# Kernel optimization log

Hardware: AMD Instinct MI355X
Metric: run time of the kernel (lower is better)

Reference implementation:

```python
import jax, jax.numpy as jnp
import numpy as np

B, S, DM, H = 4, 4096, 1024, 16
HD = DM // H  # 64


def setup_inputs() -> dict:
    key = jax.random.key(0)
    ks = jax.random.split(key, 9)
    sc = 0.02
    x = jax.random.normal(ks[0], (B, S, DM), dtype=jnp.float32)
    Wq = jax.random.normal(ks[1], (DM, DM), dtype=jnp.float32) * sc
    bq = jnp.zeros((DM,), dtype=jnp.float32)
    Wk = jax.random.normal(ks[2], (DM, HD), dtype=jnp.float32) * sc
    bk = jnp.zeros((HD,), dtype=jnp.float32)
    Wv = jax.random.normal(ks[3], (DM, HD), dtype=jnp.float32) * sc
    bv = jnp.zeros((HD,), dtype=jnp.float32)
    Wo = jax.random.normal(ks[4], (DM, DM), dtype=jnp.float32) * sc
    bo = jnp.zeros((DM,), dtype=jnp.float32)
    return {"x": x, "Wq": Wq, "bq": bq, "Wk": Wk, "bk": bk,
            "Wv": Wv, "bv": bv, "Wo": Wo, "bo": bo}


def reference(x, Wq, bq, Wk, bk, Wv, bv, Wo, bo):
    b, s, _ = x.shape
    q = (x @ Wq + bq).reshape(b, s, H, HD)          # [B,S,H,D]
    k = (x @ Wk + bk)                                # [B,S,D] (single KV head)
    v = (x @ Wv + bv)                                # [B,S,D]
    # Faithful to source: k/v expanded over head axis, matmul over last two
    # dims of [B,S,H,D] -> scores are per-token head-vs-head: [B,S,H,H].
    k_e = jnp.broadcast_to(k[:, :, None, :], (b, s, H, HD))
    v_e = jnp.broadcast_to(v[:, :, None, :], (b, s, H, HD))
    scores = jnp.einsum('bshd,bsgd->bshg', q, k_e) / jnp.sqrt(jnp.float32(HD))
    attn = jax.nn.softmax(scores, axis=-1)           # uniform (scores const over g)
    out = jnp.einsum('bshg,bsgd->bshd', attn, v_e)   # [B,S,H,D]
    return out.reshape(b, s, DM) @ Wo + bo
```

## Files before the change

### kernel.cpp

```cpp
#include <hip/hip_runtime.h>

#define M_TOTAL 16384
#define DMODEL  1024
#define HDIM    64
#define NHEAD   16

typedef _Float16 half8 __attribute__((ext_vector_type(8)));
typedef float    f32x4 __attribute__((ext_vector_type(4)));

__global__ __launch_bounds__(256) void prep_kernel(const float* __restrict__ Wv,
                                                   const float* __restrict__ Wo,
                                                   _Float16* __restrict__ WvT,
                                                   _Float16* __restrict__ WosumT) {
    const int t = blockIdx.x * 256 + threadIdx.x;
    {
        const int d = t & 63, k = t >> 6;
        WvT[d * DMODEL + k] = (_Float16)Wv[k * HDIM + d];
    }
    {
        const int n = t & 1023, d = t >> 10;
        float s = 0.f;
        #pragma unroll
        for (int h = 0; h < NHEAD; ++h) s += Wo[(h * HDIM + d) * DMODEL + n];
        WosumT[n * HDIM + d] = (_Float16)s;
    }
}

__global__ __launch_bounds__(256) void vproj_kernel(const float* __restrict__ X,
                                                    const float* __restrict__ bv,
                                                    const _Float16* __restrict__ WvT,
                                                    _Float16* __restrict__ V) {
    const int tid = threadIdx.x;
    const int l   = tid & 63;
    const int w   = tid >> 6;
    const int lr  = l & 15;
    const int lk  = l >> 4;
    const int m0  = (blockIdx.x * 4 + w) * 16;

    const float* xrow = X + (size_t)(m0 + lr) * DMODEL + lk * 8;

    f32x4 acc[4] = {};
    float4 abuf[4][2];
    #pragma unroll
    for (int s = 0; s < 4; ++s) {
        abuf[s][0] = *(const float4*)(xrow + s * 32);
        abuf[s][1] = *(const float4*)(xrow + s * 32 + 4);
    }
    #pragma unroll 4
    for (int s = 0; s < 32; ++s) {
        const int slot = s & 3;
        const float4 x0 = abuf[slot][0];
        const float4 x1 = abuf[slot][1];
        if (s < 28) {
            abuf[slot][0] = *(const float4*)(xrow + (s + 4) * 32);
            abuf[slot][1] = *(const float4*)(xrow + (s + 4) * 32 + 4);
        }
        union { _Float16 h[8]; half8 v; } pk;
        pk.h[0] = (_Float16)x0.x; pk.h[1] = (_Float16)x0.y;
        pk.h[2] = (_Float16)x0.z; pk.h[3] = (_Float16)x0.w;
        pk.h[4] = (_Float16)x1.x; pk.h[5] = (_Float16)x1.y;
        pk.h[6] = (_Float16)x1.z; pk.h[7] = (_Float16)x1.w;
        #pragma unroll
        for (int n4 = 0; n4 < 4; ++n4) {
            const half8 b = *(const half8*)&WvT[(size_t)(n4 * 16 + lr) * DMODEL + s * 32 + lk * 8];
            acc[n4] = __builtin_amdgcn_mfma_f32_16x16x32_f16(pk.v, b, acc[n4], 0, 0, 0);
        }
    }
    #pragma unroll
    for (int n4 = 0; n4 < 4; ++n4) {
        const float bvv = bv[n4 * 16 + lr];
        #pragma unroll
        for (int j = 0; j < 4; ++j)
            V[(size_t)(m0 + lk * 4 + j) * HDIM + n4 * 16 + lr] = (_Float16)(acc[n4][j] + bvv);
    }
}

__global__ __launch_bounds__(256) void oproj_kernel(const _Float16* __restrict__ V,
                                                    const float* __restrict__ bo,
                                                    const _Float16* __restrict__ WosumT,
                                                    float* __restrict__ Out) {
    const int tid = threadIdx.x;
    const int l   = tid & 63;
    const int w   = tid >> 6;
    const int lr  = l & 15;
    const int lk  = l >> 4;
    const int m0  = blockIdx.x * 16;

    const _Float16* vp = V + (size_t)(m0 + lr) * HDIM + lk * 8;
    const half8 a0 = *(const half8*)vp;
    const half8 a1 = *(const half8*)(vp + 32);

    #pragma unroll 4
    for (int nf = 0; nf < 16; ++nf) {
        const int n0 = w * 256 + nf * 16;
        const half8 b0 = *(const half8*)&WosumT[(size_t)(n0 + lr) * HDIM + lk * 8];
        const half8 b1 = *(const half8*)&WosumT[(size_t)(n0 + lr) * HDIM + 32 + lk * 8];
        f32x4 o = {};
        o = __builtin_amdgcn_mfma_f32_16x16x32_f16(a0, b0, o, 0, 0, 0);
        o = __builtin_amdgcn_mfma_f32_16x16x32_f16(a1, b1, o, 0, 0, 0);
        const float bov = bo[n0 + lr];
        #pragma unroll
        for (int j = 0; j < 4; ++j)
            Out[(size_t)(m0 + lk * 4 + j) * DMODEL + n0 + lr] = o[j] + bov;
    }
}

extern "C" void kernel_launch(void* const* d_in, const int* in_sizes, int n_in,
                              void* d_out, int out_size, void* d_ws, size_t ws_size,
                              hipStream_t stream) {
    const float* x  = (const float*)d_in[0];
    const float* Wv = (const float*)d_in[5];
    const float* bv = (const float*)d_in[6];
    const float* Wo = (const float*)d_in[7];
    const float* bo = (const float*)d_in[8];

    _Float16* WvT    = (_Float16*)d_ws;
    _Float16* WosumT = (_Float16*)((char*)d_ws + 64 * 1024 * 2);
    _Float16* V      = (_Float16*)((char*)d_ws + 256 * 1024);
    float*    out    = (float*)d_out;

    prep_kernel<<<256, 256, 0, stream>>>(Wv, Wo, WvT, WosumT);
    vproj_kernel<<<M_TOTAL / 64, 256, 0, stream>>>(x, bv, WvT, V);
    oproj_kernel<<<M_TOTAL / 16, 256, 0, stream>>>(V, bo, WosumT, out);
}
```

Before: 62.03 us.

## Split V-projection K dimension across waves and blocks with atomic reduction

Result: slower. 72.70 us (+17.2%).

```diff
diff --git a/kernel.cpp b/kernel.cpp
--- a/kernel.cpp
+++ b/kernel.cpp
@@ -11,7 +11,8 @@
 __global__ __launch_bounds__(256) void prep_kernel(const float* __restrict__ Wv,
                                                    const float* __restrict__ Wo,
                                                    _Float16* __restrict__ WvT,
-                                                   _Float16* __restrict__ WosumT) {
+                                                   _Float16* __restrict__ WosumT,
+                                                   float* __restrict__ Vg) {
     const int t = blockIdx.x * 256 + threadIdx.x;
     {
         const int d = t & 63, k = t >> 6;
@@ -24,80 +25,109 @@
         for (int h = 0; h < NHEAD; ++h) s += Wo[(h * HDIM + d) * DMODEL + n];
         WosumT[n * HDIM + d] = (_Float16)s;
     }
+    {
+        f32x4 z = {};
+        float* p = Vg + (size_t)t * 16;
+        *(f32x4*)(p) = z; *(f32x4*)(p + 4) = z;
+        *(f32x4*)(p + 8) = z; *(f32x4*)(p + 12) = z;
+    }
 }
 
-__global__ __launch_bounds__(256) void vproj_kernel(const float* __restrict__ X,
-                                                    const float* __restrict__ bv,
-                                                    const _Float16* __restrict__ WvT,
-                                                    _Float16* __restrict__ V) {
+#define VP_S 68
+
+__global__ __launch_bounds__(256, 8) void vproj_kernel(const float* __restrict__ X,
+                                                       const _Float16* __restrict__ WvT,
+                                                       float* __restrict__ Vg) {
+    __shared__ float Vp[4][16][VP_S];
+
     const int tid = threadIdx.x;
     const int l   = tid & 63;
     const int w   = tid >> 6;
     const int lr  = l & 15;
     const int lk  = l >> 4;
-    const int m0  = (blockIdx.x * 4 + w) * 16;
+    const int m0  = (blockIdx.x >> 1) * 16;
+    const int ks0 = (blockIdx.x & 1) * 512 + w * 128;
 
-    const float* xrow = X + (size_t)(m0 + lr) * DMODEL + lk * 8;
-
-    f32x4 acc[4] = {};
-    float4 abuf[4][2];
+    const float* xp = X + (size_t)(m0 + lr) * DMODEL + ks0 + lk * 8;
+    f32x4 xb[8];
     #pragma unroll
     for (int s = 0; s < 4; ++s) {
-        abuf[s][0] = *(const float4*)(xrow + s * 32);
-        abuf[s][1] = *(const float4*)(xrow + s * 32 + 4);
+        xb[2 * s]     = *(const f32x4*)(xp + s * 32);
+        xb[2 * s + 1] = *(const f32x4*)(xp + s * 32 + 4);
     }
-    #pragma unroll 4
-    for (int s = 0; s < 32; ++s) {
-        const int slot = s & 3;
-        const float4 x0 = abuf[slot][0];
-        const float4 x1 = abuf[slot][1];
-        if (s < 28) {
-            abuf[slot][0] = *(const float4*)(xrow + (s + 4) * 32);
-            abuf[slot][1] = *(const float4*)(xrow + (s + 4) * 32 + 4);
+    f32x4 acc[4] = {};
+    #pragma unroll
+    for (int s = 0; s < 4; ++s) {
+        union { _Float16 h[8]; half8 v; } pk;
+        #pragma unroll
+        for (int j = 0; j < 4; ++j) {
+            pk.h[j]     = (_Float16)xb[2 * s][j];
+            pk.h[4 + j] = (_Float16)xb[2 * s + 1][j];
         }
-        union { _Float16 h[8]; half8 v; } pk;
-        pk.h[0] = (_Float16)x0.x; pk.h[1] = (_Float16)x0.y;
-        pk.h[2] = (_Float16)x0.z; pk.h[3] = (_Float16)x0.w;
-        pk.h[4] = (_Float16)x1.x; pk.h[5] = (_Float16)x1.y;
-        pk.h[6] = (_Float16)x1.z; pk.h[7] = (_Float16)x1.w;
         #pragma unroll
         for (int n4 = 0; n4 < 4; ++n4) {
-            const half8 b = *(const half8*)&WvT[(size_t)(n4 * 16 + lr) * DMODEL + s * 32 + lk * 8];
+            const half8 b = *(const half8*)&WvT[(size_t)(n4 * 16 + lr) * DMODEL + ks0 + s * 32 + lk * 8];
             acc[n4] = __builtin_amdgcn_mfma_f32_16x16x32_f16(pk.v, b, acc[n4], 0, 0, 0);
         }
     }
     #pragma unroll
-    for (int n4 = 0; n4 < 4; ++n4) {
-        const float bvv = bv[n4 * 16 + lr];
+    for (int n4 = 0; n4 < 4; ++n4)
         #pragma unroll
         for (int j = 0; j < 4; ++j)
-            V[(size_t)(m0 + lk * 4 + j) * HDIM + n4 * 16 + lr] = (_Float16)(acc[n4][j] + bvv);
-    }
+            Vp[w][lk * 4 + j][n4 * 16 + lr] = acc[n4][j];
+    __syncthreads();
+
+    const int idx = tid * 4;
+    const int r   = idx >> 6;
+    const int c   = idx & 63;
+    f32x4 s4 = {};
+    #pragma unroll
+    for (int p = 0; p < 4; ++p) s4 += *(const f32x4*)&Vp[p][r][c];
+    float* vg = &Vg[(size_t)(m0 + r) * HDIM + c];
+    atomicAdd(vg + 0, s4[0]); atomicAdd(vg + 1, s4[1]);
+    atomicAdd(vg + 2, s4[2]); atomicAdd(vg + 3, s4[3]);
 }
 
-__global__ __launch_bounds__(256) void oproj_kernel(const _Float16* __restrict__ V,
-                                                    const float* __restrict__ bo,
-                                                    const _Float16* __restrict__ WosumT,
-                                                    float* __restrict__ Out) {
+__global__ __launch_bounds__(256, 8) void oproj_kernel(const float* __restrict__ Vg,
+                                                       const float* __restrict__ bv,
+                                                       const float* __restrict__ bo,
+                                                       const _Float16* __restrict__ WosumT,
+                                                       float* __restrict__ Out) {
     const int tid = threadIdx.x;
     const int l   = tid & 63;
     const int w   = tid >> 6;
     const int lr  = l & 15;
     const int lk  = l >> 4;
-    const int m0  = blockIdx.x * 16;
+    const int m0  = (blockIdx.x >> 1) * 16;
+    const int nb  = (blockIdx.x & 1) * 512 + w * 128;
 
-    const _Float16* vp = V + (size_t)(m0 + lr) * HDIM + lk * 8;
-    const half8 a0 = *(const half8*)vp;
-    const half8 a1 = *(const half8*)(vp + 32);
+    const float* vp = Vg + (size_t)(m0 + lr) * HDIM + lk * 8;
+    const f32x4 v0 = *(const f32x4*)(vp);
+    const f32x4 v1 = *(const f32x4*)(vp + 4);
+    const f32x4 v2 = *(const f32x4*)(vp + 32);
+    const f32x4 v3 = *(const f32x4*)(vp + 36);
+    const f32x4 b0 = *(const f32x4*)&bv[lk * 8];
+    const f32x4 b1 = *(const f32x4*)&bv[lk * 8 + 4];
+    const f32x4 b2 = *(const f32x4*)&bv[32 + lk * 8];
+    const f32x4 b3 = *(const f32x4*)&bv[32 + lk * 8 + 4];
+
+    union { _Float16 h[8]; half8 v; } A0, A1;
+    #pragma unroll
+    for (int j = 0; j < 4; ++j) {
+        A0.h[j]     = (_Float16)(v0[j] + b0[j]);
+        A0.h[4 + j] = (_Float16)(v1[j] + b1[j]);
+        A1.h[j]     = (_Float16)(v2[j] + b2[j]);
+        A1.h[4 + j] = (_Float16)(v3[j] + b3[j]);
+    }
 
     #pragma unroll 4
-    for (int nf = 0; nf < 16; ++nf) {
-        const int n0 = w * 256 + nf * 16;
-        const half8 b0 = *(const half8*)&WosumT[(size_t)(n0 + lr) * HDIM + lk * 8];
-        const half8 b1 = *(const half8*)&WosumT[(size_t)(n0 + lr) * HDIM + 32 + lk * 8];
+    for (int g = 0; g < 8; ++g) {
+        const int n0 = nb + g * 16;
+        const half8 w0 = *(const half8*)&WosumT[(size_t)(n0 + lr) * HDIM + lk * 8];
+        const half8 w1 = *(const half8*)&WosumT[(size_t)(n0 + lr) * HDIM + 32 + lk * 8];
         f32x4 o = {};
-        o = __builtin_amdgcn_mfma_f32_16x16x32_f16(a0, b0, o, 0, 0, 0);
-        o = __builtin_amdgcn_mfma_f32_16x16x32_f16(a1, b1, o, 0, 0, 0);
+        o = __builtin_amdgcn_mfma_f32_16x16x32_f16(A0.v, w0, o, 0, 0, 0);
+        o = __builtin_amdgcn_mfma_f32_16x16x32_f16(A1.v, w1, o, 0, 0, 0);
         const float bov = bo[n0 + lr];
         #pragma unroll
         for (int j = 0; j < 4; ++j)
@@ -116,10 +146,10 @@
 
     _Float16* WvT    = (_Float16*)d_ws;
     _Float16* WosumT = (_Float16*)((char*)d_ws + 64 * 1024 * 2);
-    _Float16* V      = (_Float16*)((char*)d_ws + 256 * 1024);
+    float*    Vg     = (float*)((char*)d_ws + 256 * 1024);
     float*    out    = (float*)d_out;
 
-    prep_kernel<<<256, 256, 0, stream>>>(Wv, Wo, WvT, WosumT);
-    vproj_kernel<<<M_TOTAL / 64, 256, 0, stream>>>(x, bv, WvT, V);
-    oproj_kernel<<<M_TOTAL / 16, 256, 0, stream>>>(V, bo, WosumT, out);
+    prep_kernel<<<256, 256, 0, stream>>>(Wv, Wo, WvT, WosumT, Vg);
+    vproj_kernel<<<2048, 256, 0, stream>>>(x, WvT, Vg);
+    oproj_kernel<<<2048, 256, 0, stream>>>(Vg, bv, bo, WosumT, out);
 }
```

## Split V projection K-dimension across 8 waves with LDS reduction; widen oproj grid

Applied to the files above, without the earlier changes.

New measurement: 61.64 us. Within noise of the previous version (-0.6%).

```diff
diff --git a/kernel.cpp b/kernel.cpp
--- a/kernel.cpp
+++ b/kernel.cpp
@@ -7,6 +7,7 @@
 
 typedef _Float16 half8 __attribute__((ext_vector_type(8)));
 typedef float    f32x4 __attribute__((ext_vector_type(4)));
+typedef float    f32x2 __attribute__((ext_vector_type(2)));
 
 __global__ __launch_bounds__(256) void prep_kernel(const float* __restrict__ Wv,
                                                    const float* __restrict__ Wo,
@@ -26,78 +27,101 @@
     }
 }
 
-__global__ __launch_bounds__(256) void vproj_kernel(const float* __restrict__ X,
-                                                    const float* __restrict__ bv,
-                                                    const _Float16* __restrict__ WvT,
-                                                    _Float16* __restrict__ V) {
-    const int tid = threadIdx.x;
-    const int l   = tid & 63;
-    const int w   = tid >> 6;
-    const int lr  = l & 15;
-    const int lk  = l >> 4;
-    const int m0  = (blockIdx.x * 4 + w) * 16;
+#define VP_S 68
 
-    const float* xrow = X + (size_t)(m0 + lr) * DMODEL + lk * 8;
+__global__ __launch_bounds__(512, 4) void vproj_kernel(const float* __restrict__ X,
+                                                       const float* __restrict__ bv,
+                                                       const _Float16* __restrict__ WvT,
+                                                       _Float16* __restrict__ V) {
+    __shared__ float Vp[8][16][VP_S];
 
-    f32x4 acc[4] = {};
-    float4 abuf[4][2];
-    #pragma unroll
-    for (int s = 0; s < 4; ++s) {
-        abuf[s][0] = *(const float4*)(xrow + s * 32);
-        abuf[s][1] = *(const float4*)(xrow + s * 32 + 4);
-    }
-    #pragma unroll 4
-    for (int s = 0; s < 32; ++s) {
-        const int slot = s & 3;
-        const float4 x0 = abuf[slot][0];
-        const float4 x1 = abuf[slot][1];
-        if (s < 28) {
-            abuf[slot][0] = *(const float4*)(xrow + (s + 4) * 32);
-            abuf[slot][1] = *(const float4*)(xrow + (s + 4) * 32 + 4);
-        }
-        union { _Float16 h[8]; half8 v; } pk;
-        pk.h[0] = (_Float16)x0.x; pk.h[1] = (_Float16)x0.y;
-        pk.h[2] = (_Float16)x0.z; pk.h[3] = (_Float16)x0.w;
-        pk.h[4] = (_Float16)x1.x; pk.h[5] = (_Float16)x1.y;
-        pk.h[6] = (_Float16)x1.z; pk.h[7] = (_Float16)x1.w;
-        #pragma unroll
-        for (int n4 = 0; n4 < 4; ++n4) {
-            const half8 b = *(const half8*)&WvT[(size_t)(n4 * 16 + lr) * DMODEL + s * 32 + lk * 8];
-            acc[n4] = __builtin_amdgcn_mfma_f32_16x16x32_f16(pk.v, b, acc[n4], 0, 0, 0);
-        }
-    }
-    #pragma unroll
-    for (int n4 = 0; n4 < 4; ++n4) {
-        const float bvv = bv[n4 * 16 + lr];
-        #pragma unroll
-        for (int j = 0; j < 4; ++j)
-            V[(size_t)(m0 + lk * 4 + j) * HDIM + n4 * 16 + lr] = (_Float16)(acc[n4][j] + bvv);
-    }
-}
-
-__global__ __launch_bounds__(256) void oproj_kernel(const _Float16* __restrict__ V,
-                                                    const float* __restrict__ bo,
-                                                    const _Float16* __restrict__ WosumT,
-                                                    float* __restrict__ Out) {
     const int tid = threadIdx.x;
     const int l   = tid & 63;
     const int w   = tid >> 6;
     const int lr  = l & 15;
     const int lk  = l >> 4;
     const int m0  = blockIdx.x * 16;
+    const int k0  = w * 128;
+
+    const float* xp = X + (size_t)(m0 + lr) * DMODEL + k0 + lk * 8;
+    f32x4 xb[8];
+    #pragma unroll
+    for (int s = 0; s < 4; ++s) {
+        xb[2 * s]     = *(const f32x4*)(xp + s * 32);
+        xb[2 * s + 1] = *(const f32x4*)(xp + s * 32 + 4);
+    }
+    half8 Bf[4][4];
+    #pragma unroll
+    for (int n4 = 0; n4 < 4; ++n4)
+        #pragma unroll
+        for (int s = 0; s < 4; ++s)
+            Bf[n4][s] = *(const half8*)&WvT[(size_t)(n4 * 16 + lr) * DMODEL + k0 + s * 32 + lk * 8];
+
+    f32x4 acc[4] = {};
+    #pragma unroll
+    for (int s = 0; s < 4; ++s) {
+        union { _Float16 h[8]; half8 v; } pk;
+        #pragma unroll
+        for (int j = 0; j < 4; ++j) {
+            pk.h[j]     = (_Float16)xb[2 * s][j];
+            pk.h[4 + j] = (_Float16)xb[2 * s + 1][j];
+        }
+        #pragma unroll
+        for (int n4 = 0; n4 < 4; ++n4)
+            acc[n4] = __builtin_amdgcn_mfma_f32_16x16x32_f16(pk.v, Bf[n4][s], acc[n4], 0, 0, 0);
+    }
+    #pragma unroll
+    for (int n4 = 0; n4 < 4; ++n4)
+        #pragma unroll
+        for (int j = 0; j < 4; ++j)
+            Vp[w][lk * 4 + j][n4 * 16 + lr] = acc[n4][j];
+    __syncthreads();
+
+    const int idx = tid * 2;
+    const int r   = idx >> 6;
+    const int c   = idx & 63;
+    f32x2 s2 = {};
+    #pragma unroll
+    for (int p = 0; p < 8; ++p) s2 += *(const f32x2*)&Vp[p][r][c];
+    s2 += *(const f32x2*)&bv[c];
+    union { _Float16 h[2]; unsigned int u; } o;
+    o.h[0] = (_Float16)s2[0];
+    o.h[1] = (_Float16)s2[1];
+    *(unsigned int*)&V[(size_t)(m0 + r) * HDIM + c] = o.u;
+}
+
+__global__ __launch_bounds__(256, 8) void oproj_kernel(const _Float16* __restrict__ V,
+                                                       const float* __restrict__ bo,
+                                                       const _Float16* __restrict__ WosumT,
+                                                       float* __restrict__ Out) {
+    const int tid = threadIdx.x;
+    const int l   = tid & 63;
+    const int w   = tid >> 6;
+    const int lr  = l & 15;
+    const int lk  = l >> 4;
+    const int m0  = (blockIdx.x >> 1) * 16;
+    const int nb  = (blockIdx.x & 1) * 512 + w * 128;
 
     const _Float16* vp = V + (size_t)(m0 + lr) * HDIM + lk * 8;
     const half8 a0 = *(const half8*)vp;
     const half8 a1 = *(const half8*)(vp + 32);
 
-    #pragma unroll 4
-    for (int nf = 0; nf < 16; ++nf) {
-        const int n0 = w * 256 + nf * 16;
-        const half8 b0 = *(const half8*)&WosumT[(size_t)(n0 + lr) * HDIM + lk * 8];
-        const half8 b1 = *(const half8*)&WosumT[(size_t)(n0 + lr) * HDIM + 32 + lk * 8];
+    const _Float16* wb = &WosumT[(size_t)(nb + lr) * HDIM];
+    half8 b0 = *(const half8*)(wb + lk * 8);
+    half8 b1 = *(const half8*)(wb + 32 + lk * 8);
+
+    #pragma unroll
+    for (int g = 0; g < 8; ++g) {
+        const half8 c0 = b0, c1 = b1;
+        if (g < 7) {
+            const _Float16* wn = wb + (size_t)(g + 1) * 16 * HDIM;
+            b0 = *(const half8*)(wn + lk * 8);
+            b1 = *(const half8*)(wn + 32 + lk * 8);
+        }
         f32x4 o = {};
-        o = __builtin_amdgcn_mfma_f32_16x16x32_f16(a0, b0, o, 0, 0, 0);
-        o = __builtin_amdgcn_mfma_f32_16x16x32_f16(a1, b1, o, 0, 0, 0);
+        o = __builtin_amdgcn_mfma_f32_16x16x32_f16(a0, c0, o, 0, 0, 0);
+        o = __builtin_amdgcn_mfma_f32_16x16x32_f16(a1, c1, o, 0, 0, 0);
+        const int n0 = nb + g * 16;
         const float bov = bo[n0 + lr];
         #pragma unroll
         for (int j = 0; j < 4; ++j)
@@ -120,6 +144,6 @@
     float*    out    = (float*)d_out;
 
     prep_kernel<<<256, 256, 0, stream>>>(Wv, Wo, WvT, WosumT);
-    vproj_kernel<<<M_TOTAL / 64, 256, 0, stream>>>(x, bv, WvT, V);
-    oproj_kernel<<<M_TOTAL / 16, 256, 0, stream>>>(V, bo, WosumT, out);
+    vproj_kernel<<<M_TOTAL / 16, 512, 0, stream>>>(x, bv, WvT, V);
+    oproj_kernel<<<2048, 256, 0, stream>>>(V, bo, WosumT, out);
 }
```
